# Optimization experiments

Hardware: AMD Instinct MI355X
Metric: run time of the kernel (lower is better)

Reference implementation:

```python
import jax, jax.numpy as jnp
import numpy as np

B = 8_388_608   # total windows (batch_size)
C = 4096        # number of unique channels
SEG = B // C    # windows per channel (contiguous)


def setup_inputs() -> dict:
    key = jax.random.key(0)
    output = jax.random.normal(key, (B,), dtype=jnp.float32)
    # contiguous channel ids: every channel in [0, C) present, sorted
    ch_ids = (jnp.arange(B, dtype=jnp.int32) // SEG).astype(jnp.int32)
    # target must be constant within each channel (module reads target[mask][0])
    target = (ch_ids % 2).astype(jnp.float32)
    return {"output": output, "target": target, "ch_ids": ch_ids}


def reference(output, target, ch_ids):
    # BCE branch of ChannelLoss: per-channel mean of sigmoid probs, then BCELoss
    probs = jax.nn.sigmoid(output)                                   # (B,)
    sums = jax.ops.segment_sum(probs, ch_ids, num_segments=C)        # (C,)
    counts = jax.ops.segment_sum(jnp.ones_like(probs), ch_ids, num_segments=C)
    ch_outs = sums / counts                                          # per-channel mean prob
    # first target of each channel (targets constant per channel)
    ch_targets = target[jnp.arange(C) * SEG]                         # (C,)
    # nn.BCELoss with reduction='mean'; clamp log like torch (>= -100)
    log_p = jnp.maximum(jnp.log(ch_outs), -100.0)
    log_1mp = jnp.maximum(jnp.log1p(-ch_outs), -100.0)
    loss = -jnp.mean(ch_targets * log_p + (1.0 - ch_targets) * log_1mp)
    return loss
```

## Files before the change

kernel.cpp:

```cpp
#include <hip/hip_runtime.h>
#include <math.h>

#define C_CH        4096
#define SEG_W       2048
#define CH_PER_BLK  4
#define BLKS1       (C_CH / CH_PER_BLK)

__device__ __forceinline__ float sigmoid_fast(float x) {
    return __builtin_amdgcn_rcpf(1.0f + __expf(-x));
}

__global__ __launch_bounds__(256) void channel_bce_stage1(
    const float* __restrict__ output,
    const float* __restrict__ target,
    float* __restrict__ ch_term)
{
    const int tid = threadIdx.x;
    const float4* base =
        reinterpret_cast<const float4*>(output + (size_t)blockIdx.x * (CH_PER_BLK * SEG_W));

    float4 v[8];
#pragma unroll
    for (int k = 0; k < 8; ++k)
        v[k] = base[k * 256 + tid];

    float acc[CH_PER_BLK] = {0.f, 0.f, 0.f, 0.f};
#pragma unroll
    for (int k = 0; k < 8; ++k) {
        const int j = k >> 1;
        acc[j] += sigmoid_fast(v[k].x);
        acc[j] += sigmoid_fast(v[k].y);
        acc[j] += sigmoid_fast(v[k].z);
        acc[j] += sigmoid_fast(v[k].w);
    }

#pragma unroll
    for (int j = 0; j < CH_PER_BLK; ++j)
#pragma unroll
        for (int off = 32; off > 0; off >>= 1)
            acc[j] += __shfl_down(acc[j], off, 64);

    __shared__ float wsum[4][CH_PER_BLK];
    if ((tid & 63) == 0) {
        const int w = tid >> 6;
#pragma unroll
        for (int j = 0; j < CH_PER_BLK; ++j)
            wsum[w][j] = acc[j];
    }
    __syncthreads();

    if (tid < CH_PER_BLK) {
        const float sum  = wsum[0][tid] + wsum[1][tid] + wsum[2][tid] + wsum[3][tid];
        const float mean = sum * (1.0f / (float)SEG_W);
        const int   c    = blockIdx.x * CH_PER_BLK + tid;
        const float t    = target[(size_t)c * SEG_W];
        const float log_p   = fmaxf(logf(mean),    -100.0f);
        const float log_1mp = fmaxf(log1pf(-mean), -100.0f);
        ch_term[c] = t * log_p + (1.0f - t) * log_1mp;
    }
}

__global__ __launch_bounds__(256) void channel_bce_stage2(
    const float* __restrict__ ch_term,
    float* __restrict__ out)
{
    const int tid = threadIdx.x;
    float acc = 0.0f;
#pragma unroll
    for (int i = 0; i < C_CH / 256; ++i)
        acc += ch_term[i * 256 + tid];

#pragma unroll
    for (int off = 32; off > 0; off >>= 1)
        acc += __shfl_down(acc, off, 64);

    __shared__ float wsum[4];
    if ((tid & 63) == 0) wsum[tid >> 6] = acc;
    __syncthreads();

    if (tid == 0) {
        const float s = wsum[0] + wsum[1] + wsum[2] + wsum[3];
        out[0] = -s * (1.0f / (float)C_CH);
    }
}

extern "C" void kernel_launch(void* const* d_in, const int* in_sizes, int n_in,
                              void* d_out, int out_size, void* d_ws, size_t ws_size,
                              hipStream_t stream) {
    const float* output = (const float*)d_in[0];
    const float* target = (const float*)d_in[1];
    float* ch_term = (float*)d_ws;
    float* out     = (float*)d_out;

    channel_bce_stage1<<<BLKS1, 256, 0, stream>>>(output, target, ch_term);
    channel_bce_stage2<<<1, 256, 0, stream>>>(ch_term, out);
}
```

Baseline: 11.80 us.

## Fuse stage-two reduction into stage one via packed fixed-point atomic counter

Removes the separate single-block reduction kernel. Each block converts its partial BCE term to biased fixed-point and packs it with an arrival counter into a single 64-bit atomicAdd, and the last block to arrive writes the final loss. This drops one kernel launch and a global round trip, but adds a memset on the stream plus a single contended atomic address, and fixed-point quantization at a scale of 2^30 could overflow or lose precision if per-block terms are large.

```diff
diff --git a/kernel.cpp b/kernel.cpp
--- a/kernel.cpp
+++ b/kernel.cpp
@@ -6,14 +6,20 @@
 #define CH_PER_BLK  4
 #define BLKS1       (C_CH / CH_PER_BLK)
 
+#define SCALE_F     1073741824.0f
+#define BIAS_LL     (512LL << 30)
+#define CNT_SHIFT   53
+#define SUM_MASK    ((1ULL << CNT_SHIFT) - 1)
+
 __device__ __forceinline__ float sigmoid_fast(float x) {
     return __builtin_amdgcn_rcpf(1.0f + __expf(-x));
 }
 
-__global__ __launch_bounds__(256) void channel_bce_stage1(
+__global__ __launch_bounds__(256) void channel_bce_fused(
     const float* __restrict__ output,
     const float* __restrict__ target,
-    float* __restrict__ ch_term)
+    unsigned long long* __restrict__ acc,
+    float* __restrict__ out)
 {
     const int tid = threadIdx.x;
     const float4* base =
@@ -24,28 +30,29 @@
     for (int k = 0; k < 8; ++k)
         v[k] = base[k * 256 + tid];
 
-    float acc[CH_PER_BLK] = {0.f, 0.f, 0.f, 0.f};
+    float s[CH_PER_BLK] = {0.f, 0.f, 0.f, 0.f};
 #pragma unroll
     for (int k = 0; k < 8; ++k) {
         const int j = k >> 1;
-        acc[j] += sigmoid_fast(v[k].x);
-        acc[j] += sigmoid_fast(v[k].y);
-        acc[j] += sigmoid_fast(v[k].z);
-        acc[j] += sigmoid_fast(v[k].w);
+        s[j] += sigmoid_fast(v[k].x);
+        s[j] += sigmoid_fast(v[k].y);
+        s[j] += sigmoid_fast(v[k].z);
+        s[j] += sigmoid_fast(v[k].w);
     }
 
 #pragma unroll
     for (int j = 0; j < CH_PER_BLK; ++j)
 #pragma unroll
         for (int off = 32; off > 0; off >>= 1)
-            acc[j] += __shfl_down(acc[j], off, 64);
+            s[j] += __shfl_down(s[j], off, 64);
 
     __shared__ float wsum[4][CH_PER_BLK];
+    __shared__ float term[CH_PER_BLK];
     if ((tid & 63) == 0) {
         const int w = tid >> 6;
 #pragma unroll
         for (int j = 0; j < CH_PER_BLK; ++j)
-            wsum[w][j] = acc[j];
+            wsum[w][j] = s[j];
     }
     __syncthreads();
 
@@ -56,31 +63,23 @@
         const float t    = target[(size_t)c * SEG_W];
         const float log_p   = fmaxf(logf(mean),    -100.0f);
         const float log_1mp = fmaxf(log1pf(-mean), -100.0f);
-        ch_term[c] = t * log_p + (1.0f - t) * log_1mp;
+        term[tid] = t * log_p + (1.0f - t) * log_1mp;
     }
-}
-
-__global__ __launch_bounds__(256) void channel_bce_stage2(
-    const float* __restrict__ ch_term,
-    float* __restrict__ out)
-{
-    const int tid = threadIdx.x;
-    float acc = 0.0f;
-#pragma unroll
-    for (int i = 0; i < C_CH / 256; ++i)
-        acc += ch_term[i * 256 + tid];
-
-#pragma unroll
-    for (int off = 32; off > 0; off >>= 1)
-        acc += __shfl_down(acc, off, 64);
-
-    __shared__ float wsum[4];
-    if ((tid & 63) == 0) wsum[tid >> 6] = acc;
     __syncthreads();
 
     if (tid == 0) {
-        const float s = wsum[0] + wsum[1] + wsum[2] + wsum[3];
-        out[0] = -s * (1.0f / (float)C_CH);
+        const float partial = (term[0] + term[1]) + (term[2] + term[3]);
+        const long long fx  = llrintf(partial * SCALE_F);
+        const unsigned long long my =
+            (1ULL << CNT_SHIFT) + (unsigned long long)(fx + BIAS_LL);
+        const unsigned long long old = atomicAdd(acc, my);
+        if ((old >> CNT_SHIFT) == (unsigned long long)(BLKS1 - 1)) {
+            const unsigned long long total = old + my;
+            const long long sum_biased = (long long)(total & SUM_MASK);
+            const long long sum_fx     = sum_biased - (long long)BLKS1 * BIAS_LL;
+            const double loss = -((double)sum_fx * (1.0 / 1073741824.0)) / (double)C_CH;
+            out[0] = (float)loss;
+        }
     }
 }
 
@@ -89,9 +88,9 @@
                               hipStream_t stream) {
     const float* output = (const float*)d_in[0];
     const float* target = (const float*)d_in[1];
-    float* ch_term = (float*)d_ws;
-    float* out     = (float*)d_out;
+    unsigned long long* acc = (unsigned long long*)d_ws;
+    float* out = (float*)d_out;
 
-    channel_bce_stage1<<<BLKS1, 256, 0, stream>>>(output, target, ch_term);
-    channel_bce_stage2<<<1, 256, 0, stream>>>(ch_term, out);
+    hipMemsetAsync(d_ws, 0, sizeof(unsigned long long), stream);
+    channel_bce_fused<<<BLKS1, 256, 0, stream>>>(output, target, acc, out);
 }
```

Result: slower. 25.52 us (+116.2%).
